# Kernel optimization log

Hardware: AMD Instinct MI355X
Metric: run time of the kernel (lower is better)

The kernel has to match this reference:

```python
import jax, jax.numpy as jnp
import numpy as np

B, T, D, H = 32, 1024, 512, 256  # batch, seq_len, input_size, lstm hidden per direction (2H == D)


def _lstm_dir(x_tbd, W_ih, W_hh, b):
    """Single-direction LSTM over time-major input [T, B, D] -> hidden states [T, B, H].
    PyTorch gate order: i, f, g, o."""
    xg = jnp.einsum('tbd,gd->tbg', x_tbd, W_ih) + b  # precompute input projections [T,B,4H]
    h0 = jnp.zeros((x_tbd.shape[1], W_hh.shape[1]), x_tbd.dtype)

    def step(carry, xt):
        h, c = carry
        g = xt + h @ W_hh.T
        i, f, gg, o = jnp.split(g, 4, axis=-1)
        c = jax.nn.sigmoid(f) * c + jax.nn.sigmoid(i) * jnp.tanh(gg)
        h = jax.nn.sigmoid(o) * jnp.tanh(c)
        return (h, c), h

    _, hs = jax.lax.scan(step, (h0, h0), xg)
    return hs


def setup_inputs() -> dict:
    key = jax.random.key(0)
    ks = jax.random.split(key, 10)
    s = 0.05
    # padding mask: 1 (True) for padding positions, built from random valid lengths
    lengths = jax.random.randint(ks[1], (B,), T // 2, T)
    x_mask = jnp.arange(T)[None, :] >= lengths[:, None]  # bool [B, T]
    return {
        'x': jax.random.normal(ks[0], (B, T, D), jnp.float32),
        'x_mask': x_mask,
        'W_ih_f': jax.random.normal(ks[2], (4 * H, D), jnp.float32) * s,
        'W_hh_f': jax.random.normal(ks[3], (4 * H, H), jnp.float32) * s,
        'b_f': jnp.zeros((4 * H,), jnp.float32),
        'W_ih_b': jax.random.normal(ks[4], (4 * H, D), jnp.float32) * s,
        'W_hh_b': jax.random.normal(ks[5], (4 * H, H), jnp.float32) * s,
        'b_b': jnp.zeros((4 * H,), jnp.float32),
        'W_l': jax.random.normal(ks[6], (D, D), jnp.float32) * s,
    }


def reference(x, x_mask, W_ih_f, W_hh_f, b_f, W_ih_b, W_hh_b, b_b, W_l):
    # BiRNN encode: 1-layer bidirectional LSTM, concat directions -> [B, T, 2H] == [B, T, D]
    xt = jnp.swapaxes(x, 0, 1)  # [T, B, D]
    h_f = _lstm_dir(xt, W_ih_f, W_hh_f, b_f)
    h_b = _lstm_dir(xt[::-1], W_ih_b, W_hh_b, b_b)[::-1]
    xe = jnp.swapaxes(jnp.concatenate([h_f, h_b], axis=-1), 0, 1)  # [B, T, D]

    # Bilinear self-attention: L = (x W_l^T) x^T, mask padded query rows, softmax, weighted sum
    proj = xe @ W_l.T  # [B, T, D]
    L = jnp.einsum('bid,bjd->bij', proj, xe)  # [B, T, T]
    L = jnp.where(x_mask[:, :, None], jnp.float32(-1e30), L)
    A = jax.nn.softmax(L, axis=-1)
    return jnp.einsum('bij,bjd->bid', A, xe)  # [B, T, D]
```

## Files before the change

### kernel.cpp

```cpp
#include <hip/hip_runtime.h>
#include <math.h>

#define T_SEQ 1024
#define B_SZ  32
#define D_SZ  512
#define H_SZ  256

#define BM 64
#define BN 64
#define BK 16

__global__ __launch_bounds__(256)
void gemm_nt(const float* __restrict__ A, const float* __restrict__ W,
             const float* __restrict__ bias, float* __restrict__ C,
             int M, int N, int K,
             long long sA, long long sW, long long sC)
{
    int z = blockIdx.z;
    A += (size_t)z * sA; W += (size_t)z * sW; C += (size_t)z * sC;
    int n0 = blockIdx.x * BN;
    int m0 = blockIdx.y * BM;
    int tid = threadIdx.x;
    int tm = tid >> 4, tn = tid & 15;

    __shared__ float As[BK][BM + 4];
    __shared__ float Ws[BK][BN + 4];

    float acc[4][4] = {};

    int lc = tid & 15;
    int lr = tid >> 4;

    for (int k0 = 0; k0 < K; k0 += BK) {
        #pragma unroll
        for (int i = 0; i < 4; ++i) {
            int r = lr + 16 * i;
            As[lc][r] = A[(size_t)(m0 + r) * K + k0 + lc];
            Ws[lc][r] = W[(size_t)(n0 + r) * K + k0 + lc];
        }
        __syncthreads();
        #pragma unroll
        for (int kk = 0; kk < BK; ++kk) {
            float4 a4 = *(const float4*)&As[kk][tm * 4];
            float4 b4 = *(const float4*)&Ws[kk][tn * 4];
            float a[4] = {a4.x, a4.y, a4.z, a4.w};
            float b[4] = {b4.x, b4.y, b4.z, b4.w};
            #pragma unroll
            for (int i = 0; i < 4; ++i)
                #pragma unroll
                for (int j = 0; j < 4; ++j)
                    acc[i][j] = fmaf(a[i], b[j], acc[i][j]);
        }
        __syncthreads();
    }

    float bb[4] = {0.f, 0.f, 0.f, 0.f};
    if (bias) {
        #pragma unroll
        for (int j = 0; j < 4; ++j) bb[j] = bias[n0 + tn * 4 + j];
    }
    #pragma unroll
    for (int i = 0; i < 4; ++i) {
        int m = m0 + tm * 4 + i;
        float4 o;
        o.x = acc[i][0] + bb[0];
        o.y = acc[i][1] + bb[1];
        o.z = acc[i][2] + bb[2];
        o.w = acc[i][3] + bb[3];
        *(float4*)&C[(size_t)m * N + n0 + tn * 4] = o;
    }
}

__global__ __launch_bounds__(256)
void gemm_nn(const float* __restrict__ A, const float* __restrict__ B,
             float* __restrict__ C, int M, int N, int K,
             long long sA, long long sB, long long sC)
{
    int z = blockIdx.z;
    A += (size_t)z * sA; B += (size_t)z * sB; C += (size_t)z * sC;
    int n0 = blockIdx.x * BN;
    int m0 = blockIdx.y * BM;
    int tid = threadIdx.x;
    int tm = tid >> 4, tn = tid & 15;

    __shared__ float As[BK][BM + 4];
    __shared__ float Bs[BK][BN + 4];

    float acc[4][4] = {};

    int lc = tid & 15;
    int lr = tid >> 4;
    int br = tid >> 6;
    int bc = tid & 63;

    for (int k0 = 0; k0 < K; k0 += BK) {
        #pragma unroll
        for (int i = 0; i < 4; ++i) {
            int r = lr + 16 * i;
            As[lc][r] = A[(size_t)(m0 + r) * K + k0 + lc];
        }
        #pragma unroll
        for (int i = 0; i < 4; ++i) {
            int r = br + 4 * i;
            Bs[r][bc] = B[(size_t)(k0 + r) * N + n0 + bc];
        }
        __syncthreads();
        #pragma unroll
        for (int kk = 0; kk < BK; ++kk) {
            float4 a4 = *(const float4*)&As[kk][tm * 4];
            float4 b4 = *(const float4*)&Bs[kk][tn * 4];
            float a[4] = {a4.x, a4.y, a4.z, a4.w};
            float b[4] = {b4.x, b4.y, b4.z, b4.w};
            #pragma unroll
            for (int i = 0; i < 4; ++i)
                #pragma unroll
                for (int j = 0; j < 4; ++j)
                    acc[i][j] = fmaf(a[i], b[j], acc[i][j]);
        }
        __syncthreads();
    }
    #pragma unroll
    for (int i = 0; i < 4; ++i) {
        int m = m0 + tm * 4 + i;
        float4 o;
        o.x = acc[i][0]; o.y = acc[i][1]; o.z = acc[i][2]; o.w = acc[i][3];
        *(float4*)&C[(size_t)m * N + n0 + tn * 4] = o;
    }
}

__device__ __forceinline__ unsigned int f2bf(float f)
{
    unsigned int u = __float_as_uint(f);
    return (u + 0x7fffu + ((u >> 16) & 1u)) >> 16;
}

__global__ __launch_bounds__(256)
void pack_whh_bf16(const float* __restrict__ Wf, const float* __restrict__ Wb,
                   uint4* __restrict__ Wpf, uint4* __restrict__ Wpb)
{
    int idx = blockIdx.x * 256 + threadIdx.x;
    int u = idx & (H_SZ - 1);
    int p = idx >> 8;
    uint4 a, b;
    unsigned int* pa = (unsigned int*)&a;
    unsigned int* pb = (unsigned int*)&b;
    #pragma unroll
    for (int g = 0; g < 4; ++g) {
        size_t row = (size_t)(g * H_SZ + u) * H_SZ;
        pa[g] = f2bf(Wf[row + 2 * p]) | (f2bf(Wf[row + 2 * p + 1]) << 16);
        pb[g] = f2bf(Wb[row + 2 * p]) | (f2bf(Wb[row + 2 * p + 1]) << 16);
    }
    Wpf[idx] = a;
    Wpb[idx] = b;
}

__global__ __launch_bounds__(1024)
void lstm_bf16(const float* __restrict__ xgA, const uint4* __restrict__ WpA,
               const float* __restrict__ xgB, const uint4* __restrict__ WpB,
               float* __restrict__ xe, int d0, int fused)
{
    int i = blockIdx.x;
    int b, dir;
    if (fused) {
        int j = i & 7, m = i >> 3;
        dir = j >> 2;
        b   = (j & 3) * 8 + m;
    } else {
        b   = (i & 3) * 8 + (i >> 2);
        dir = d0;
    }
    const float* xg = dir ? xgB : xgA;
    const uint4* Wp = dir ? WpB : WpA;

    int tid   = threadIdx.x;
    int u     = tid & (H_SZ - 1);
    int slice = tid >> 8;
    int p0    = slice << 5;

    __shared__ float  hs[H_SZ];
    __shared__ float4 part[4][H_SZ];

    uint4 wres[16];
    {
        const uint4* wb = Wp + (size_t)p0 * H_SZ + u;
        #pragma unroll
        for (int q = 0; q < 16; ++q) wres[q] = wb[q * H_SZ];
    }
    const uint4* wstream = Wp + (size_t)(p0 + 16) * H_SZ + u;

    if (tid < H_SZ) hs[tid] = 0.f;
    float c = 0.f;
    __syncthreads();

    for (int s = 0; s < T_SEQ; ++s) {
        int t = dir ? (T_SEQ - 1 - s) : s;

        float xi = 0.f, xf = 0.f, xgv = 0.f, xo = 0.f;
        if (tid < H_SZ) {
            const float* row = xg + ((size_t)b * T_SEQ + t) * (4 * H_SZ);
            xi  = row[u];
            xf  = row[H_SZ + u];
            xgv = row[2 * H_SZ + u];
            xo  = row[3 * H_SZ + u];
        }

        float4 acc; acc.x = 0.f; acc.y = 0.f; acc.z = 0.f; acc.w = 0.f;

        #define DOT_PAIR(WQ, P)                                             \
        {                                                                   \
            float2 hp = *(const float2*)&hs[2 * (P)];                       \
            const unsigned int* wc = (const unsigned int*)&(WQ);            \
            _Pragma("unroll")                                               \
            for (int g = 0; g < 4; ++g) {                                   \
                float wlo = __uint_as_float(wc[g] << 16);                   \
                float whi = __uint_as_float(wc[g] & 0xffff0000u);           \
                ((float*)&acc)[g] =                                         \
                    fmaf(whi, hp.y, fmaf(wlo, hp.x, ((float*)&acc)[g]));    \
            }                                                               \
        }

        #pragma unroll
        for (int q = 0; q < 16; ++q) {
            DOT_PAIR(wres[q], p0 + q);
        }
        #pragma unroll
        for (int q = 0; q < 16; ++q) {
            int qr = (q + s) & 15;
            uint4 wq = wstream[(size_t)qr * H_SZ];
            DOT_PAIR(wq, p0 + 16 + qr);
        }
        #undef DOT_PAIR

        part[slice][u] = acc;
        __syncthreads();

        if (tid < H_SZ) {
            float4 pp0 = part[0][u], pp1 = part[1][u], pp2 = part[2][u], pp3 = part[3][u];
            float ai = xi  + pp0.x + pp1.x + pp2.x + pp3.x;
            float af = xf  + pp0.y + pp1.y + pp2.y + pp3.y;
            float ag = xgv + pp0.z + pp1.z + pp2.z + pp3.z;
            float ao = xo  + pp0.w + pp1.w + pp2.w + pp3.w;
            float ig = 1.f / (1.f + __expf(-ai));
            float fg = 1.f / (1.f + __expf(-af));
            float gg = tanhf(ag);
            float og = 1.f / (1.f + __expf(-ao));
            c = fg * c + ig * gg;
            float h = og * tanhf(c);
            hs[u] = h;
            xe[((size_t)b * T_SEQ + t) * D_SZ + dir * H_SZ + u] = h;
        }
        __syncthreads();
    }
}

__global__ __launch_bounds__(256)
void softmax_rows(float* __restrict__ L, const void* __restrict__ maskraw)
{
    const unsigned char* mu8 = (const unsigned char*)maskraw;
    const int*           mi32 = (const int*)maskraw;
    bool layout_u8 = (mu8[1023] != 0);

    int lane = threadIdx.x & 63;
    int wid  = threadIdx.x >> 6;
    int row  = (blockIdx.x << 2) + wid;
    float* p = L + (size_t)row * T_SEQ;

    int mval = layout_u8 ? (int)mu8[row] : mi32[row];

    if (mval != 0) {
        const float inv = 1.0f / (float)T_SEQ;
        for (int j = lane; j < T_SEQ; j += 64) p[j] = inv;
        return;
    }

    float v[16];
    float m = -1e30f;
    #pragma unroll
    for (int u = 0; u < 16; ++u) {
        v[u] = p[lane + (u << 6)];
        m = fmaxf(m, v[u]);
    }
    #pragma unroll
    for (int s = 32; s; s >>= 1) m = fmaxf(m, __shfl_xor(m, s, 64));

    float sum = 0.f;
    #pragma unroll
    for (int u = 0; u < 16; ++u) {
        v[u] = __expf(v[u] - m);
        sum += v[u];
    }
    #pragma unroll
    for (int s = 32; s; s >>= 1) sum += __shfl_xor(sum, s, 64);

    float inv = 1.0f / sum;
    #pragma unroll
    for (int u = 0; u < 16; ++u) p[lane + (u << 6)] = v[u] * inv;
}

extern "C" void kernel_launch(void* const* d_in, const int* in_sizes, int n_in,
                              void* d_out, int out_size, void* d_ws, size_t ws_size,
                              hipStream_t stream)
{
    const float* x     = (const float*)d_in[0];
    const void*  xmask = d_in[1];
    const float* Wih_f = (const float*)d_in[2];
    const float* Whh_f = (const float*)d_in[3];
    const float* b_f   = (const float*)d_in[4];
    const float* Wih_b = (const float*)d_in[5];
    const float* Whh_b = (const float*)d_in[6];
    const float* b_b   = (const float*)d_in[7];
    const float* W_l   = (const float*)d_in[8];
    float* out = (float*)d_out;

    char* ws = (char*)d_ws;
    const size_t SZ_XE = (size_t)B_SZ * T_SEQ * D_SZ * sizeof(float);
    const size_t SZ_XG = (size_t)B_SZ * T_SEQ * 4 * H_SZ * sizeof(float);
    bool fused = ws_size >= SZ_XE + 2 * SZ_XG;

    float* xe   = (float*)(ws);
    float* xg_f = (float*)(ws + SZ_XE);
    float* xg_b = fused ? (float*)(ws + SZ_XE + SZ_XG)
                        : xg_f;
    float* L    = xg_f;

    uint4* Wpf = (uint4*)out;
    uint4* Wpb = (uint4*)out + 128 * H_SZ;
    float* proj = out;

    const int MT = B_SZ * T_SEQ;
    const long long sTD = (long long)T_SEQ * D_SZ;
    const long long sTT = (long long)T_SEQ * T_SEQ;

    pack_whh_bf16<<<dim3((128 * H_SZ) / 256), dim3(256), 0, stream>>>(
        Whh_f, Whh_b, Wpf, Wpb);

    if (fused) {
        gemm_nt<<<dim3((4 * H_SZ) / BN, MT / BM, 1), dim3(256), 0, stream>>>(
            x, Wih_f, b_f, xg_f, MT, 4 * H_SZ, D_SZ, 0, 0, 0);
        gemm_nt<<<dim3((4 * H_SZ) / BN, MT / BM, 1), dim3(256), 0, stream>>>(
            x, Wih_b, b_b, xg_b, MT, 4 * H_SZ, D_SZ, 0, 0, 0);
        lstm_bf16<<<dim3(2 * B_SZ), dim3(1024), 0, stream>>>(
            xg_f, Wpf, xg_b, Wpb, xe, 0, 1);
    } else {
        gemm_nt<<<dim3((4 * H_SZ) / BN, MT / BM, 1), dim3(256), 0, stream>>>(
            x, Wih_f, b_f, xg_f, MT, 4 * H_SZ, D_SZ, 0, 0, 0);
        lstm_bf16<<<dim3(B_SZ), dim3(1024), 0, stream>>>(
            xg_f, Wpf, xg_f, Wpf, xe, 0, 0);
        gemm_nt<<<dim3((4 * H_SZ) / BN, MT / BM, 1), dim3(256), 0, stream>>>(
            x, Wih_b, b_b, xg_b, MT, 4 * H_SZ, D_SZ, 0, 0, 0);
        lstm_bf16<<<dim3(B_SZ), dim3(1024), 0, stream>>>(
            xg_b, Wpb, xg_b, Wpb, xe, 1, 0);
    }

    gemm_nt<<<dim3(D_SZ / BN, MT / BM, 1), dim3(256), 0, stream>>>(
        xe, W_l, nullptr, proj, MT, D_SZ, D_SZ, 0, 0, 0);

    gemm_nt<<<dim3(T_SEQ / BN, T_SEQ / BM, B_SZ), dim3(256), 0, stream>>>(
        proj, xe, nullptr, L, T_SEQ, T_SEQ, D_SZ, sTD, sTD, sTT);

    softmax_rows<<<dim3(MT / 4), dim3(256), 0, stream>>>(L, xmask);

    gemm_nn<<<dim3(D_SZ / BN, T_SEQ / BM, B_SZ), dim3(256), 0, stream>>>(
        L, xe, out, T_SEQ, D_SZ, T_SEQ, sTT, sTD, sTD);
}
```

Before: 17.04 ms.

## Run attention GEMMs on bf16 MFMA with hi/lo split for fp32 accuracy

Replaces the three fp32 SIMT attention GEMMs (projection, scores, weighted sum) with an MFMA 16x16x32 bf16 kernel. Each fp32 operand is split into bf16 high and low parts, and three MFMA products are summed to approximate fp32 accuracy. New conversion and transpose kernels prepare the split operands, and the workspace layout is reorganised to hold them. This adds extra conversion passes and memory traffic, and precision is slightly below true fp32.

```diff
diff --git a/kernel.cpp b/kernel.cpp
--- a/kernel.cpp
+++ b/kernel.cpp
@@ -5,6 +5,25 @@
 #define B_SZ  32
 #define D_SZ  512
 #define H_SZ  256
+
+typedef unsigned short u16;
+typedef short v8bf __attribute__((ext_vector_type(8)));
+typedef float v4f  __attribute__((ext_vector_type(4)));
+
+__device__ __forceinline__ unsigned int f2bf(float f)
+{
+    unsigned int u = __float_as_uint(f);
+    return (u + 0x7fffu + ((u >> 16) & 1u)) >> 16;
+}
+__device__ __forceinline__ u16 f2bfu(float f)
+{
+    unsigned int u = __float_as_uint(f);
+    return (u16)((u + 0x7fffu + ((u >> 16) & 1u)) >> 16);
+}
+__device__ __forceinline__ float bfu2f(u16 h)
+{
+    return __uint_as_float(((unsigned int)h) << 16);
+}
 
 #define BM 64
 #define BN 64
@@ -128,10 +147,175 @@
     }
 }
 
-__device__ __forceinline__ unsigned int f2bf(float f)
-{
-    unsigned int u = __float_as_uint(f);
-    return (u + 0x7fffu + ((u >> 16) & 1u)) >> 16;
+#define LDK 40
+
+template<int MODE>
+__global__ __launch_bounds__(256)
+void gemm_mf(const void* __restrict__ Aa, const void* __restrict__ Ab,
+             const u16* __restrict__ Bh0, const u16* __restrict__ Bl0,
+             float* __restrict__ C, u16* __restrict__ Chi, u16* __restrict__ Clo,
+             int M, int N, int K,
+             long long sA, long long sB, long long sC)
+{
+    int z  = blockIdx.z;
+    int n0 = blockIdx.x * 128;
+    int m0 = blockIdx.y * 128;
+    int t  = threadIdx.x;
+
+    const u16* Bh = Bh0 + (size_t)z * sB;
+    const u16* Bl = Bl0 + (size_t)z * sB;
+
+    __shared__ u16 sAh[128][LDK];
+    __shared__ u16 sAl[128][LDK];
+    __shared__ u16 sBh[128][LDK];
+    __shared__ u16 sBl[128][LDK];
+
+    int lane = t & 63, wid = t >> 6;
+    int wm = (wid & 1) << 6;
+    int wn = (wid >> 1) << 6;
+    int fr  = lane & 15;
+    int fko = (lane >> 4) << 3;
+
+    v4f acc[4][4];
+    #pragma unroll
+    for (int i = 0; i < 4; ++i)
+        #pragma unroll
+        for (int j = 0; j < 4; ++j)
+            acc[i][j] = (v4f){0.f, 0.f, 0.f, 0.f};
+
+    for (int k0 = 0; k0 < K; k0 += 32) {
+        if (MODE != 2) {
+            const u16* Ah = (const u16*)Aa + (size_t)z * sA;
+            const u16* Al = (const u16*)Ab + (size_t)z * sA;
+            #pragma unroll
+            for (int i = 0; i < 2; ++i) {
+                int s = t + (i << 8);
+                int r = s >> 2, kc = (s & 3) << 3;
+                *(uint4*)&sAh[r][kc] = *(const uint4*)&Ah[(size_t)(m0 + r) * K + k0 + kc];
+                *(uint4*)&sAl[r][kc] = *(const uint4*)&Al[(size_t)(m0 + r) * K + k0 + kc];
+            }
+        } else {
+            const float* Af = (const float*)Aa + (size_t)z * sA;
+            #pragma unroll
+            for (int i = 0; i < 4; ++i) {
+                int s = t + (i << 8);
+                int r = s >> 3, kc = (s & 7) << 2;
+                float4 v = *(const float4*)&Af[(size_t)(m0 + r) * K + k0 + kc];
+                u16 h0 = f2bfu(v.x), h1 = f2bfu(v.y), h2 = f2bfu(v.z), h3 = f2bfu(v.w);
+                ushort4 hh; hh.x = h0; hh.y = h1; hh.z = h2; hh.w = h3;
+                ushort4 ll;
+                ll.x = f2bfu(v.x - bfu2f(h0));
+                ll.y = f2bfu(v.y - bfu2f(h1));
+                ll.z = f2bfu(v.z - bfu2f(h2));
+                ll.w = f2bfu(v.w - bfu2f(h3));
+                *(ushort4*)&sAh[r][kc] = hh;
+                *(ushort4*)&sAl[r][kc] = ll;
+            }
+        }
+        #pragma unroll
+        for (int i = 0; i < 2; ++i) {
+            int s = t + (i << 8);
+            int r = s >> 2, kc = (s & 3) << 3;
+            *(uint4*)&sBh[r][kc] = *(const uint4*)&Bh[(size_t)(n0 + r) * K + k0 + kc];
+            *(uint4*)&sBl[r][kc] = *(const uint4*)&Bl[(size_t)(n0 + r) * K + k0 + kc];
+        }
+        __syncthreads();
+
+        v8bf bh[4], bl[4];
+        #pragma unroll
+        for (int ni = 0; ni < 4; ++ni) {
+            bh[ni] = *(const v8bf*)&sBh[wn + ni * 16 + fr][fko];
+            bl[ni] = *(const v8bf*)&sBl[wn + ni * 16 + fr][fko];
+        }
+        #pragma unroll
+        for (int mi = 0; mi < 4; ++mi) {
+            v8bf ah = *(const v8bf*)&sAh[wm + mi * 16 + fr][fko];
+            v8bf al = *(const v8bf*)&sAl[wm + mi * 16 + fr][fko];
+            #pragma unroll
+            for (int ni = 0; ni < 4; ++ni) {
+                acc[mi][ni] = __builtin_amdgcn_mfma_f32_16x16x32_bf16(ah, bh[ni], acc[mi][ni], 0, 0, 0);
+                acc[mi][ni] = __builtin_amdgcn_mfma_f32_16x16x32_bf16(al, bh[ni], acc[mi][ni], 0, 0, 0);
+                acc[mi][ni] = __builtin_amdgcn_mfma_f32_16x16x32_bf16(ah, bl[ni], acc[mi][ni], 0, 0, 0);
+            }
+        }
+        __syncthreads();
+    }
+
+    int orow = (lane >> 4) << 2;
+    int ocol = lane & 15;
+    if (MODE == 1) {
+        #pragma unroll
+        for (int mi = 0; mi < 4; ++mi) {
+            #pragma unroll
+            for (int r = 0; r < 4; ++r) {
+                int m = m0 + wm + mi * 16 + orow + r;
+                #pragma unroll
+                for (int ni = 0; ni < 4; ++ni) {
+                    int n = n0 + wn + ni * 16 + ocol;
+                    float v = acc[mi][ni][r];
+                    u16 h = f2bfu(v);
+                    Chi[(size_t)m * N + n] = h;
+                    Clo[(size_t)m * N + n] = f2bfu(v - bfu2f(h));
+                }
+            }
+        }
+    } else {
+        float* Cz = C + (size_t)z * sC;
+        #pragma unroll
+        for (int mi = 0; mi < 4; ++mi) {
+            #pragma unroll
+            for (int r = 0; r < 4; ++r) {
+                int m = m0 + wm + mi * 16 + orow + r;
+                #pragma unroll
+                for (int ni = 0; ni < 4; ++ni) {
+                    int n = n0 + wn + ni * 16 + ocol;
+                    Cz[(size_t)m * N + n] = acc[mi][ni][r];
+                }
+            }
+        }
+    }
+}
+
+__global__ __launch_bounds__(256)
+void convert_split(const float4* __restrict__ in,
+                   ushort4* __restrict__ hi, ushort4* __restrict__ lo)
+{
+    size_t i = (size_t)blockIdx.x * 256 + threadIdx.x;
+    float4 v = in[i];
+    ushort4 h, l;
+    h.x = f2bfu(v.x); l.x = f2bfu(v.x - bfu2f(h.x));
+    h.y = f2bfu(v.y); l.y = f2bfu(v.y - bfu2f(h.y));
+    h.z = f2bfu(v.z); l.z = f2bfu(v.z - bfu2f(h.z));
+    h.w = f2bfu(v.w); l.w = f2bfu(v.w - bfu2f(h.w));
+    hi[i] = h;
+    lo[i] = l;
+}
+
+__global__ __launch_bounds__(256)
+void transpose_split_xe(const float* __restrict__ xe,
+                        u16* __restrict__ Th, u16* __restrict__ Tl)
+{
+    int b = blockIdx.z;
+    const float* X = xe + (size_t)b * T_SEQ * D_SZ;
+    u16* TH = Th + (size_t)b * T_SEQ * D_SZ;
+    u16* TL = Tl + (size_t)b * T_SEQ * D_SZ;
+    int t0 = blockIdx.x << 5, d0 = blockIdx.y << 5;
+
+    __shared__ float tile[32][33];
+    int tx = threadIdx.x & 31, ty = threadIdx.x >> 5;
+
+    #pragma unroll
+    for (int i = 0; i < 4; ++i)
+        tile[ty + (i << 3)][tx] = X[(size_t)(t0 + ty + (i << 3)) * D_SZ + d0 + tx];
+    __syncthreads();
+    #pragma unroll
+    for (int i = 0; i < 4; ++i) {
+        int dd = ty + (i << 3);
+        float v = tile[tx][dd];
+        u16 h = f2bfu(v);
+        TH[(size_t)(d0 + dd) * T_SEQ + t0 + tx] = h;
+        TL[(size_t)(d0 + dd) * T_SEQ + t0 + tx] = f2bfu(v - bfu2f(h));
+    }
 }
 
 __global__ __launch_bounds__(256)
@@ -313,35 +497,71 @@
     float* out = (float*)d_out;
 
     char* ws = (char*)d_ws;
+    const size_t MB1 = (size_t)1 << 20;
     const size_t SZ_XE = (size_t)B_SZ * T_SEQ * D_SZ * sizeof(float);
     const size_t SZ_XG = (size_t)B_SZ * T_SEQ * 4 * H_SZ * sizeof(float);
     bool fused = ws_size >= SZ_XE + 2 * SZ_XG;
 
-    float* xe   = (float*)(ws);
-    float* xg_f = (float*)(ws + SZ_XE);
-    float* xg_b = fused ? (float*)(ws + SZ_XE + SZ_XG)
-                        : xg_f;
-    float* L    = xg_f;
-
-    uint4* Wpf = (uint4*)out;
-    uint4* Wpb = (uint4*)out + 128 * H_SZ;
-    float* proj = out;
-
     const int MT = B_SZ * T_SEQ;
     const long long sTD = (long long)T_SEQ * D_SZ;
     const long long sTT = (long long)T_SEQ * T_SEQ;
 
+    uint4* Wpf = (uint4*)d_out;
+    uint4* Wpb = (uint4*)d_out + 128 * H_SZ;
+
     pack_whh_bf16<<<dim3((128 * H_SZ) / 256), dim3(256), 0, stream>>>(
         Whh_f, Whh_b, Wpf, Wpb);
 
     if (fused) {
+        float* xe    = (float*)(ws);
+        float* xg_f  = (float*)(ws + 64 * MB1);
+        float* xg_b  = (float*)(ws + 192 * MB1);
+        float* L     = xg_f;
+        u16* xe_hi   = (u16*)(ws + 192 * MB1);
+        u16* xe_lo   = (u16*)(ws + 224 * MB1);
+        u16* pj_hi   = (u16*)(ws + 256 * MB1);
+        u16* pj_lo   = (u16*)(ws + 288 * MB1);
+        u16* xT_hi   = pj_hi;
+        u16* xT_lo   = pj_lo;
+        u16* Wl_hi   = (u16*)((char*)d_out + 2 * MB1);
+        u16* Wl_lo   = (u16*)((char*)d_out + 2 * MB1 + (MB1 >> 1));
+
         gemm_nt<<<dim3((4 * H_SZ) / BN, MT / BM, 1), dim3(256), 0, stream>>>(
             x, Wih_f, b_f, xg_f, MT, 4 * H_SZ, D_SZ, 0, 0, 0);
         gemm_nt<<<dim3((4 * H_SZ) / BN, MT / BM, 1), dim3(256), 0, stream>>>(
             x, Wih_b, b_b, xg_b, MT, 4 * H_SZ, D_SZ, 0, 0, 0);
+
         lstm_bf16<<<dim3(2 * B_SZ), dim3(1024), 0, stream>>>(
             xg_f, Wpf, xg_b, Wpb, xe, 0, 1);
+
+        convert_split<<<dim3((MT * D_SZ) / 1024), dim3(256), 0, stream>>>(
+            (const float4*)xe, (ushort4*)xe_hi, (ushort4*)xe_lo);
+        convert_split<<<dim3((D_SZ * D_SZ) / 1024), dim3(256), 0, stream>>>(
+            (const float4*)W_l, (ushort4*)Wl_hi, (ushort4*)Wl_lo);
+
+        gemm_mf<1><<<dim3(D_SZ / 128, MT / 128, 1), dim3(256), 0, stream>>>(
+            xe_hi, xe_lo, Wl_hi, Wl_lo, nullptr, pj_hi, pj_lo,
+            MT, D_SZ, D_SZ, 0, 0, 0);
+
+        gemm_mf<0><<<dim3(T_SEQ / 128, T_SEQ / 128, B_SZ), dim3(256), 0, stream>>>(
+            pj_hi, pj_lo, xe_hi, xe_lo, L, nullptr, nullptr,
+            T_SEQ, T_SEQ, D_SZ, sTD, sTD, sTT);
+
+        softmax_rows<<<dim3(MT / 4), dim3(256), 0, stream>>>(L, xmask);
+
+        transpose_split_xe<<<dim3(T_SEQ / 32, D_SZ / 32, B_SZ), dim3(256), 0, stream>>>(
+            xe, xT_hi, xT_lo);
+
+        gemm_mf<2><<<dim3(D_SZ / 128, T_SEQ / 128, B_SZ), dim3(256), 0, stream>>>(
+            L, L, xT_hi, xT_lo, out, nullptr, nullptr,
+            T_SEQ, D_SZ, T_SEQ, sTT, sTD, sTD);
     } else {
+        float* xe   = (float*)(ws);
+        float* xg_f = (float*)(ws + SZ_XE);
+        float* xg_b = xg_f;
+        float* L    = xg_f;
+        float* proj = out;
+
         gemm_nt<<<dim3((4 * H_SZ) / BN, MT / BM, 1), dim3(256), 0, stream>>>(
             x, Wih_f, b_f, xg_f, MT, 4 * H_SZ, D_SZ, 0, 0, 0);
         lstm_bf16<<<dim3(B_SZ), dim3(1024), 0, stream>>>(
@@ -350,16 +570,13 @@
             x, Wih_b, b_b, xg_b, MT, 4 * H_SZ, D_SZ, 0, 0, 0);
         lstm_bf16<<<dim3(B_SZ), dim3(1024), 0, stream>>>(
             xg_b, Wpb, xg_b, Wpb, xe, 1, 0);
-    }
-
-    gemm_nt<<<dim3(D_SZ / BN, MT / BM, 1), dim3(256), 0, stream>>>(
-        xe, W_l, nullptr, proj, MT, D_SZ, D_SZ, 0, 0, 0);
-
-    gemm_nt<<<dim3(T_SEQ / BN, T_SEQ / BM, B_SZ), dim3(256), 0, stream>>>(
-        proj, xe, nullptr, L, T_SEQ, T_SEQ, D_SZ, sTD, sTD, sTT);
-
-    softmax_rows<<<dim3(MT / 4), dim3(256), 0, stream>>>(L, xmask);
-
-    gemm_nn<<<dim3(D_SZ / BN, T_SEQ / BM, B_SZ), dim3(256), 0, stream>>>(
-        L, xe, out, T_SEQ, D_SZ, T_SEQ, sTT, sTD, sTD);
-}
+
+        gemm_nt<<<dim3(D_SZ / BN, MT / BM, 1), dim3(256), 0, stream>>>(
+            xe, W_l, nullptr, proj, MT, D_SZ, D_SZ, 0, 0, 0);
+        gemm_nt<<<dim3(T_SEQ / BN, T_SEQ / BM, B_SZ), dim3(256), 0, stream>>>(
+            proj, xe, nullptr, L, T_SEQ, T_SEQ, D_SZ, sTD, sTD, sTT);
+        softmax_rows<<<dim3(MT / 4), dim3(256), 0, stream>>>(L, xmask);
+        gemm_nn<<<dim3(D_SZ / BN, T_SEQ / BM, B_SZ), dim3(256), 0, stream>>>(
+            L, xe, out, T_SEQ, D_SZ, T_SEQ, sTT, sTD, sTD);
+    }
+}
```

Result: no change. 17.25 ms (+1.2%).
